# Kernel optimization log

Hardware: AMD Instinct MI355X
Metric: run time of the kernel (lower is better)

## Reference

```python
import jax, jax.numpy as jnp
import numpy as np

C_S = 256
C_Z = 128
C_HIDDEN = 32
NO_HEADS = 8
INF = 1000000000.0
EPS = 1e-5


def _layernorm(x, w, b):
    mu = jnp.mean(x, axis=-1, keepdims=True)
    var = jnp.var(x, axis=-1, keepdims=True)
    return (x - mu) * jax.lax.rsqrt(var + EPS) * w + b


def setup_inputs() -> dict:
    key = jax.random.key(0)
    ks = jax.random.split(key, 12)
    B, S, R = 1, 128, 256
    H, D = NO_HEADS, C_HIDDEN
    hd = H * D
    inp = {
        "s": jax.random.normal(ks[0], (B, S, R, C_S), dtype=jnp.float32),
        "z": jax.random.normal(ks[1], (B, R, R, C_Z), dtype=jnp.float32),
        "mask": jnp.ones((B, S, R), dtype=jnp.float32),
        "ln_s_w": jnp.ones((C_S,), dtype=jnp.float32),
        "ln_s_b": jnp.zeros((C_S,), dtype=jnp.float32),
        "ln_z_w": jnp.ones((C_Z,), dtype=jnp.float32),
        "ln_z_b": jnp.zeros((C_Z,), dtype=jnp.float32),
        "w_z": jax.random.normal(ks[2], (C_Z, H), dtype=jnp.float32) * 0.02,
        "w_q": jax.random.normal(ks[3], (C_S, hd), dtype=jnp.float32) * (1.0 / np.sqrt(C_S)),
        "w_k": jax.random.normal(ks[4], (C_S, hd), dtype=jnp.float32) * (1.0 / np.sqrt(C_S)),
        "w_v": jax.random.normal(ks[5], (C_S, hd), dtype=jnp.float32) * (1.0 / np.sqrt(C_S)),
        "w_g": jax.random.normal(ks[6], (C_S, hd), dtype=jnp.float32) * 0.02,
        "b_g": jnp.ones((hd,), dtype=jnp.float32),
        "w_o": jax.random.normal(ks[7], (hd, C_S), dtype=jnp.float32) * (1.0 / np.sqrt(hd)),
        "b_o": jnp.zeros((C_S,), dtype=jnp.float32),
    }
    return inp


def reference(s, z, mask, ln_s_w, ln_s_b, ln_z_w, ln_z_b, w_z, w_q, w_k, w_v, w_g, b_g, w_o, b_o):
    B, S, R, _ = s.shape
    H, D = NO_HEADS, C_HIDDEN

    s_n = _layernorm(s, ln_s_w, ln_s_b)                      # [B,S,R,C_s]
    # mask bias: [B, S, 1, 1, R]
    mask_bias = (INF * (mask - 1.0))[..., :, None, None, :]
    # pair bias: [B, 1, H, R, R]
    z_n = _layernorm(z, ln_z_w, ln_z_b)                      # [B,R,R,C_z]
    pair_bias = jnp.einsum("bqkc,ch->bhqk", z_n, w_z)[:, None]

    q = jnp.einsum("bsqc,cx->bsqx", s_n, w_q).reshape(B, S, R, H, D)
    k = jnp.einsum("bskc,cx->bskx", s_n, w_k).reshape(B, S, R, H, D)
    v = jnp.einsum("bskc,cx->bskx", s_n, w_v).reshape(B, S, R, H, D)
    q = q * (1.0 / np.sqrt(D))

    # attention logits: [B, S, H, R(q), R(k)]
    logits = jnp.einsum("bsqhd,bskhd->bshqk", q, k) + mask_bias + pair_bias
    attn = jax.nn.softmax(logits, axis=-1)
    o = jnp.einsum("bshqk,bskhd->bsqhd", attn, v).reshape(B, S, R, H * D)

    g = jax.nn.sigmoid(jnp.einsum("bsqc,cx->bsqx", s_n, w_g) + b_g)
    o = o * g
    out = jnp.einsum("bsqx,xc->bsqc", o, w_o) + b_o          # [B,S,R,C_s]
    return out
```

## Files before the change

kernel.cpp:

```cpp
#include <hip/hip_runtime.h>
#include <math.h>

#define CS 256
#define CZ 128
#define HEADS 8
#define DH 32
#define SDIM 128
#define RDIM 256
#define MROWS (SDIM*RDIM)
#define ZROWS (RDIM*RDIM)
#define EPSF 1e-5f
#define LOG2E 1.44269504088896340736f

typedef __attribute__((ext_vector_type(8))) short short8_t;
typedef __attribute__((ext_vector_type(4))) float f32x4;

__device__ __forceinline__ float waveReduceSum(float v) {
    #pragma unroll
    for (int off = 32; off > 0; off >>= 1) v += __shfl_xor(v, off, 64);
    return v;
}

__device__ __forceinline__ unsigned short f2bf(float f) {
    unsigned u = __float_as_uint(f);
    unsigned r = (u + 0x7fffu + ((u >> 16) & 1u)) >> 16;
    return (unsigned short)r;
}

__device__ __forceinline__ float bf2f(unsigned short u) {
    return __uint_as_float(((unsigned)u) << 16);
}

__device__ __forceinline__ float bflo(unsigned u) { return __uint_as_float(u << 16); }
__device__ __forceinline__ float bfhi(unsigned u) { return __uint_as_float(u & 0xffff0000u); }

__device__ __forceinline__ unsigned cvt_pk_bf16(float a, float b) {
    unsigned r;
    asm("v_cvt_pk_bf16_f32 %0, %1, %2" : "=v"(r) : "v"(a), "v"(b));
    return r;
}

__global__ __launch_bounds__(256) void ln_s_kernel(const float* __restrict__ s,
        const float* __restrict__ w, const float* __restrict__ b,
        unsigned short* __restrict__ snb) {
    int wid = threadIdx.x >> 6;
    int lane = threadIdx.x & 63;
    int row = blockIdx.x * 4 + wid;
    const float4 v = ((const float4*)(s + (size_t)row * CS))[lane];
    float sum = waveReduceSum(v.x + v.y + v.z + v.w);
    float sq  = waveReduceSum(v.x*v.x + v.y*v.y + v.z*v.z + v.w*v.w);
    float mean = sum * (1.f/CS);
    float var  = sq * (1.f/CS) - mean*mean;
    float rstd = rsqrtf(var + EPSF);
    const float4 wv = ((const float4*)w)[lane];
    const float4 bv = ((const float4*)b)[lane];
    ushort4 o;
    o.x = f2bf((v.x-mean)*rstd*wv.x + bv.x);
    o.y = f2bf((v.y-mean)*rstd*wv.y + bv.y);
    o.z = f2bf((v.z-mean)*rstd*wv.z + bv.z);
    o.w = f2bf((v.w-mean)*rstd*wv.w + bv.w);
    ((ushort4*)(snb + (size_t)row * CS))[lane] = o;
}

__global__ __launch_bounds__(256) void ln_z_pb_kernel(const float* __restrict__ z,
        const float* __restrict__ w, const float* __restrict__ b,
        const float* __restrict__ wz, unsigned short* __restrict__ pb) {
    int wid = threadIdx.x >> 6;
    int lane = threadIdx.x & 63;
    int row = blockIdx.x * 4 + wid;
    const float2 v = ((const float2*)(z + (size_t)row * CZ))[lane];
    float sum = waveReduceSum(v.x + v.y);
    float sq  = waveReduceSum(v.x*v.x + v.y*v.y);
    float mean = sum * (1.f/CZ);
    float var  = sq * (1.f/CZ) - mean*mean;
    float rstd = rsqrtf(var + EPSF);
    const float2 wv = ((const float2*)w)[lane];
    const float2 bv = ((const float2*)b)[lane];
    float n0 = (v.x-mean)*rstd*wv.x + bv.x;
    float n1 = (v.y-mean)*rstd*wv.y + bv.y;
    const float* wz0 = wz + (size_t)(lane*2) * HEADS;
    float ph[8];
    #pragma unroll
    for (int h = 0; h < 8; h++) ph[h] = n0*wz0[h] + n1*wz0[HEADS + h];
    #pragma unroll
    for (int h = 0; h < 8; h++) ph[h] = waveReduceSum(ph[h]);
    if (lane == 0) {
        #pragma unroll
        for (int h = 0; h < 8; h++)
            pb[(size_t)h*ZROWS + row] = f2bf(ph[h]);
    }
}

__global__ __launch_bounds__(256) void wconv_kernel(const float* __restrict__ wq,
        const float* __restrict__ wk, const float* __restrict__ wv,
        const float* __restrict__ wg, const float* __restrict__ wo,
        unsigned short* __restrict__ wtb, unsigned short* __restrict__ wot) {
    __shared__ float T[64][65];
    const int wi = blockIdx.z;
    const float* W = (wi==0)?wq:(wi==1)?wk:(wi==2)?wv:(wi==3)?wg:wo;
    unsigned short* O = (wi<4) ? (wtb + (size_t)wi*65536) : wot;
    const int bk = blockIdx.x * 64, bn = blockIdx.y * 64;
    const int tx = threadIdx.x & 63, tg = threadIdx.x >> 6;
    #pragma unroll
    for (int i = 0; i < 16; i++) {
        int r = tg*16 + i;
        T[r][tx] = W[(size_t)(bk+r)*256 + bn + tx];
    }
    __syncthreads();
    #pragma unroll
    for (int i = 0; i < 16; i++) {
        int r = tg*16 + i;
        O[(size_t)(bn+r)*256 + bk + tx] = f2bf(T[tx][r]);
    }
}

__global__ __launch_bounds__(256, 3) void qkvg_kernel(
        const unsigned short* __restrict__ snb,
        const unsigned short* __restrict__ wtb,
        const float* __restrict__ bg,
        unsigned short* __restrict__ qo, unsigned short* __restrict__ ko,
        unsigned short* __restrict__ vo, unsigned short* __restrict__ go) {
    __shared__ alignas(16) unsigned short As[128][64];
    __shared__ alignas(16) unsigned short Bs[128][64];
    const int bx = blockIdx.x;
    const int mblk = (bx & 7) * 32 + (bx >> 3);
    const int m0 = mblk * 128;
    const int n0 = blockIdx.y * 128;
    const int seg = n0 >> 8;
    const int nseg = n0 & 255;
    const unsigned short* wt = wtb + (size_t)seg * 65536;
    const int tid = threadIdx.x;
    const int lane = tid & 63, wid = tid >> 6;
    const int ln15 = lane & 15, g = lane >> 4;
    const int wr = wid >> 1, wc = wid & 1;
    f32x4 acc[4][4];
    #pragma unroll
    for (int i = 0; i < 4; i++)
        #pragma unroll
        for (int j = 0; j < 4; j++) acc[i][j] = (f32x4){0.f,0.f,0.f,0.f};

    for (int k0 = 0; k0 < 256; k0 += 64) {
        #pragma unroll
        for (int ci = 0; ci < 4; ci++) {
            int n = tid + ci*256;
            int r = n >> 3, sc = n & 7;
            int gc = (sc + r) & 7;
            const unsigned short* sA = &snb[(size_t)(m0+r)*256 + k0 + gc*8];
            const unsigned short* sB = &wt[(size_t)(nseg+r)*256 + k0 + gc*8];
            __builtin_amdgcn_global_load_lds(
                (const __attribute__((address_space(1))) unsigned int*)sA,
                (__attribute__((address_space(3))) unsigned int*)(&As[0][0] + (size_t)(wid*64 + ci*256)*8),
                16, 0, 0);
            __builtin_amdgcn_global_load_lds(
                (const __attribute__((address_space(1))) unsigned int*)sB,
                (__attribute__((address_space(3))) unsigned int*)(&Bs[0][0] + (size_t)(wid*64 + ci*256)*8),
                16, 0, 0);
        }
        __syncthreads();
        #pragma unroll
        for (int kk = 0; kk < 64; kk += 32) {
            short8_t a[4], b[4];
            #pragma unroll
            for (int i = 0; i < 4; i++) {
                int ga = (kk >> 3) + g;
                int ra = wr*64 + i*16 + ln15;
                int rb = wc*64 + i*16 + ln15;
                a[i] = *(const short8_t*)&As[ra][((ga - ra) & 7) * 8];
                b[i] = *(const short8_t*)&Bs[rb][((ga - rb) & 7) * 8];
            }
            #pragma unroll
            for (int i = 0; i < 4; i++)
                #pragma unroll
                for (int j = 0; j < 4; j++)
                    acc[i][j] = __builtin_amdgcn_mfma_f32_16x16x32_bf16(
                                    a[i], b[j], acc[i][j], 0, 0, 0);
        }
        __syncthreads();
    }
    #pragma unroll
    for (int i = 0; i < 4; i++) {
        #pragma unroll
        for (int r = 0; r < 4; r++) {
            int m = m0 + wr*64 + i*16 + g*4 + r;
            int ss = m >> 8, rr = m & 255;
            #pragma unroll
            for (int j = 0; j < 4; j++) {
                int col = n0 + wc*64 + j*16 + ln15;
                int lc = col & 255;
                int h = lc >> 5, d = lc & 31;
                float val = acc[i][j][r];
                size_t qidx = (((size_t)ss*HEADS + h)*RDIM + rr)*DH + d;
                if (seg == 0)      qo[qidx] = f2bf(val * 0.17677669529663687f);
                else if (seg == 1) ko[qidx] = f2bf(val);
                else if (seg == 2) vo[qidx] = f2bf(val);
                else {
                    float x = val + bg[lc];
                    go[(size_t)m*CS + lc] = f2bf(1.f / (1.f + expf(-x)));
                }
            }
        }
    }
}

__global__ __launch_bounds__(256, 2) void attn_kernel(
        const unsigned short* __restrict__ q, const unsigned short* __restrict__ k,
        const unsigned short* __restrict__ v, const unsigned short* __restrict__ pb,
        const float* __restrict__ mask, unsigned short* __restrict__ o) {
    __shared__ alignas(16) unsigned short Klds[256][40];
    __shared__ alignas(16) unsigned short Vtlds[32][264];
    __shared__ alignas(16) unsigned short PBpb[4][4096];
    __shared__ alignas(16) unsigned short Plds[4][16][72];
    __shared__ float masklds[256];

    const int sh = blockIdx.x;
    const int ss = sh >> 3, h = sh & 7;
    const int tid = threadIdx.x;
    const int lane = tid & 63, wid = tid >> 6;
    const int ln15 = lane & 15, g = lane >> 4;

    const unsigned short* kp = k + (size_t)sh * 8192;
    const unsigned short* vp = v + (size_t)sh * 8192;
    const unsigned short* pbh = pb + (size_t)h * ZROWS;
    unsigned short* pbw = &PBpb[wid][0];

    {
        const unsigned short* pbase = pbh + (size_t)(wid*64) * RDIM;
        #pragma unroll
        for (int j = 0; j < 8; j++) {
            int w = j*64 + lane;
            int n = w ^ ((w >> 5) & 7);
            const unsigned short* src = pbase + (n >> 5) * RDIM + (n & 31) * 8;
            __builtin_amdgcn_global_load_lds(
                (const __attribute__((address_space(1))) unsigned int*)src,
                (__attribute__((address_space(3))) unsigned int*)(pbw + j*512),
                16, 0, 0);
        }
    }

    #pragma unroll
    for (int i = 0; i < 4; i++) {
        int idx = tid + i*256;
        int row = idx >> 2, col = (idx & 3) * 8;
        short8_t kv8 = *(const short8_t*)&kp[(size_t)row*DH + col];
        short8_t vv8 = *(const short8_t*)&vp[(size_t)row*DH + col];
        *(short8_t*)&Klds[row][col] = kv8;
        #pragma unroll
        for (int e = 0; e < 8; e++)
            Vtlds[col+e][row] = (unsigned short)vv8[e];
    }
    masklds[tid] = 1e9f * (mask[(size_t)ss*RDIM + tid] - 1.f);

    short8_t qfr[4];
    {
        const unsigned short* qp = q + (size_t)sh * 8192;
        #pragma unroll
        for (int qt = 0; qt < 4; qt++)
            qfr[qt] = *(const short8_t*)&qp[(size_t)(wid*64 + qt*16 + ln15)*DH + g*8];
    }
    __syncthreads();

    #pragma unroll 1
    for (int qt = 0; qt < 4; qt++) {
        const int q0 = wid*64 + qt*16;
        f32x4 st[16];
        #pragma unroll
        for (int t = 0; t < 16; t++) {
            short8_t kf = *(const short8_t*)&Klds[t*16 + ln15][g*8];
            st[t] = __builtin_amdgcn_mfma_f32_16x16x32_bf16(
                        kf, qfr[qt], (f32x4){0.f,0.f,0.f,0.f}, 0, 0, 0);
        }
        asm volatile("s_waitcnt vmcnt(0)" ::: "memory");
        __builtin_amdgcn_sched_barrier(0);
        #pragma unroll
        for (int t = 0; t < 16; t++) {
            int n = ln15*32 + t*2 + (g >> 1);
            int m = n ^ (ln15 & 7);
            uint2 p2 = *(const uint2*)&pbw[m*8 + (g & 1)*4];
            float4 mk4 = *(const float4*)&masklds[t*16 + g*4];
            st[t][0] += bflo(p2.x) + mk4.x;
            st[t][1] += bfhi(p2.x) + mk4.y;
            st[t][2] += bflo(p2.y) + mk4.z;
            st[t][3] += bfhi(p2.y) + mk4.w;
        }
        float mx = -INFINITY;
        #pragma unroll
        for (int t = 0; t < 16; t++) {
            float a = fmaxf(fmaxf(st[t][0], st[t][1]), fmaxf(st[t][2], st[t][3]));
            mx = fmaxf(mx, a);
        }
        mx = fmaxf(mx, __shfl_xor(mx, 16, 64));
        mx = fmaxf(mx, __shfl_xor(mx, 32, 64));
        const float mxl = mx * LOG2E;
        float l = 0.f;
        #pragma unroll
        for (int t = 0; t < 16; t++) {
            #pragma unroll
            for (int r = 0; r < 4; r++) {
                float p = exp2f(fmaf(st[t][r], LOG2E, -mxl));
                st[t][r] = p;
                l += p;
            }
        }
        l += __shfl_xor(l, 16, 64);
        l += __shfl_xor(l, 32, 64);
        float inv = 1.f / l;
        if (qt < 3) {
            const unsigned short* pbase = pbh + (size_t)(q0 + 16) * RDIM;
            #pragma unroll
            for (int j = 0; j < 8; j++) {
                int w = j*64 + lane;
                int n = w ^ ((w >> 5) & 7);
                const unsigned short* src = pbase + (n >> 5) * RDIM + (n & 31) * 8;
                __builtin_amdgcn_global_load_lds(
                    (const __attribute__((address_space(1))) unsigned int*)src,
                    (__attribute__((address_space(3))) unsigned int*)(pbw + j*512),
                    16, 0, 0);
            }
        }
        f32x4 oacc[2];
        oacc[0] = (f32x4){0.f,0.f,0.f,0.f};
        oacc[1] = (f32x4){0.f,0.f,0.f,0.f};
        #pragma unroll
        for (int c = 0; c < 4; c++) {
            #pragma unroll
            for (int tc = 0; tc < 4; tc++) {
                int t = c*4 + tc;
                uint2 w;
                w.x = cvt_pk_bf16(st[t][0], st[t][1]);
                w.y = cvt_pk_bf16(st[t][2], st[t][3]);
                *(uint2*)&Plds[wid][ln15][tc*16 + g*4] = w;
            }
            #pragma unroll
            for (int ks = 0; ks < 2; ks++) {
                short8_t pfr = *(const short8_t*)&Plds[wid][ln15][ks*32 + g*8];
                #pragma unroll
                for (int dt = 0; dt < 2; dt++) {
                    short8_t vf = *(const short8_t*)&Vtlds[dt*16 + ln15][c*64 + ks*32 + g*8];
                    oacc[dt] = __builtin_amdgcn_mfma_f32_16x16x32_bf16(
                                   vf, pfr, oacc[dt], 0, 0, 0);
                }
            }
        }
        #pragma unroll
        for (int dt = 0; dt < 2; dt++) {
            uint2 w;
            w.x = cvt_pk_bf16(oacc[dt][0]*inv, oacc[dt][1]*inv);
            w.y = cvt_pk_bf16(oacc[dt][2]*inv, oacc[dt][3]*inv);
            *(uint2*)&Plds[wid][ln15][dt*16 + g*4] = w;
        }
        {
            int qr = lane >> 2, dc = (lane & 3) * 8;
            short8_t ov = *(const short8_t*)&Plds[wid][qr][dc];
            *(short8_t*)&o[((size_t)ss*RDIM + q0 + qr)*CS + h*DH + dc] = ov;
        }
    }
}

__global__ __launch_bounds__(256, 3) void outproj_kernel(
        const unsigned short* __restrict__ ob, const unsigned short* __restrict__ gb,
        const unsigned short* __restrict__ wot, const float* __restrict__ bo,
        float* __restrict__ out) {
    __shared__ alignas(16) unsigned short As[128][64];
    __shared__ alignas(16) unsigned short Bs[128][64];
    const int bx = blockIdx.x;
    const int mblk = (bx & 7) * 32 + (bx >> 3);
    const int m0 = mblk * 128;
    const int n0 = blockIdx.y * 128;
    const int tid = threadIdx.x;
    const int lane = tid & 63, wid = tid >> 6;
    const int ln15 = lane & 15, g = lane >> 4;
    const int wr = wid >> 1, wc = wid & 1;
    f32x4 acc[4][4];
    #pragma unroll
    for (int i = 0; i < 4; i++)
        #pragma unroll
        for (int j = 0; j < 4; j++) acc[i][j] = (f32x4){0.f,0.f,0.f,0.f};

    for (int k0 = 0; k0 < 256; k0 += 64) {
        #pragma unroll
        for (int ci = 0; ci < 4; ci++) {
            int n = tid + ci*256;
            int r = n >> 3, sc = n & 7;
            int gcb = (sc + r) & 7;
            const unsigned short* sB = &wot[(size_t)(n0+r)*256 + k0 + gcb*8];
            __builtin_amdgcn_global_load_lds(
                (const __attribute__((address_space(1))) unsigned int*)sB,
                (__attribute__((address_space(3))) unsigned int*)(&Bs[0][0] + (size_t)(wid*64 + ci*256)*8),
                16, 0, 0);
            int row = r, gc = sc;
            short8_t ov = *(const short8_t*)&ob[(size_t)(m0+row)*256 + k0 + gc*8];
            short8_t gv = *(const short8_t*)&gb[(size_t)(m0+row)*256 + k0 + gc*8];
            unsigned pr[4];
            #pragma unroll
            for (int e = 0; e < 4; e++) {
                float p0 = bf2f((unsigned short)ov[e*2+0]) * bf2f((unsigned short)gv[e*2+0]);
                float p1 = bf2f((unsigned short)ov[e*2+1]) * bf2f((unsigned short)gv[e*2+1]);
                pr[e] = cvt_pk_bf16(p0, p1);
            }
            *(uint4*)&As[row][((gc - row) & 7) * 8] = *(uint4*)pr;
        }
        __syncthreads();
        #pragma unroll
        for (int kk = 0; kk < 64; kk += 32) {
            short8_t a[4], b[4];
            #pragma unroll
            for (int i = 0; i < 4; i++) {
                int ga = (kk >> 3) + g;
                int ra = wr*64 + i*16 + ln15;
                int rb = wc*64 + i*16 + ln15;
                a[i] = *(const short8_t*)&As[ra][((ga - ra) & 7) * 8];
                b[i] = *(const short8_t*)&Bs[rb][((ga - rb) & 7) * 8];
            }
            #pragma unroll
            for (int i = 0; i < 4; i++)
                #pragma unroll
                for (int j = 0; j < 4; j++)
                    acc[i][j] = __builtin_amdgcn_mfma_f32_16x16x32_bf16(
                                    a[i], b[j], acc[i][j], 0, 0, 0);
        }
        __syncthreads();
    }
    #pragma unroll
    for (int i = 0; i < 4; i++) {
        #pragma unroll
        for (int r = 0; r < 4; r++) {
            int m = m0 + wr*64 + i*16 + g*4 + r;
            #pragma unroll
            for (int j = 0; j < 4; j++) {
                int col = n0 + wc*64 + j*16 + ln15;
                out[(size_t)m*CS + col] = acc[i][j][r] + bo[col];
            }
        }
    }
}

extern "C" void kernel_launch(void* const* d_in, const int* in_sizes, int n_in,
                              void* d_out, int out_size, void* d_ws, size_t ws_size,
                              hipStream_t stream) {
    const float* s      = (const float*)d_in[0];
    const float* z      = (const float*)d_in[1];
    const float* mask   = (const float*)d_in[2];
    const float* ln_s_w = (const float*)d_in[3];
    const float* ln_s_b = (const float*)d_in[4];
    const float* ln_z_w = (const float*)d_in[5];
    const float* ln_z_b = (const float*)d_in[6];
    const float* w_z    = (const float*)d_in[7];
    const float* w_q    = (const float*)d_in[8];
    const float* w_k    = (const float*)d_in[9];
    const float* w_v    = (const float*)d_in[10];
    const float* w_g    = (const float*)d_in[11];
    const float* b_g    = (const float*)d_in[12];
    const float* w_o    = (const float*)d_in[13];
    const float* b_o    = (const float*)d_in[14];
    float* out = (float*)d_out;
    float* ws  = (float*)d_ws;

    unsigned short* snb = (unsigned short*)ws;
    unsigned short* wtb = (unsigned short*)(ws + 4194304);
    unsigned short* wot = (unsigned short*)(ws + 4194304+131072);
    unsigned short* pbb = (unsigned short*)(ws + 4194304+131072+32768);
    float* after_pb = ws + 4194304 + 131072 + 32768 + 262144;
    unsigned short* qb  = (unsigned short*)after_pb;
    unsigned short* kb  = qb + 8388608;
    unsigned short* vb  = kb + 8388608;
    unsigned short* gbuf= vb + 8388608;
    unsigned short* obuf= gbuf + 8388608;

    ln_s_kernel<<<MROWS/4, 256, 0, stream>>>(s, ln_s_w, ln_s_b, snb);
    ln_z_pb_kernel<<<ZROWS/4, 256, 0, stream>>>(z, ln_z_w, ln_z_b, w_z, pbb);
    wconv_kernel<<<dim3(4,4,5), 256, 0, stream>>>(w_q, w_k, w_v, w_g, w_o, wtb, wot);
    qkvg_kernel<<<dim3(MROWS/128, 8), 256, 0, stream>>>(snb, wtb, b_g, qb, kb, vb, gbuf);
    attn_kernel<<<SDIM*HEADS, 256, 0, stream>>>(qb, kb, vb, pbb, mask, obuf);
    outproj_kernel<<<dim3(MROWS/128, 2), 256, 0, stream>>>(obuf, gbuf, wot, b_o, out);
}
```

Before: 174.3 us.

## Compute z pair-bias projection with MFMA and coalesced bf16 stores

Rewrites the z layernorm and pair-bias kernel so each block handles 64 rows. Each lane-group of 16 lanes owns one row, and the 128x8 projection runs as bf16 MFMA 16x16x32 instead of eight full-wave shuffle reductions per row. Results are staged in shared memory and written as 16-byte vector stores per head, replacing scattered 2-byte stores. This cuts shuffle traffic and store inefficiency, at the cost of rounding the normalized z and w_z to bf16 before the dot product.

```diff
diff --git a/kernel.cpp b/kernel.cpp
--- a/kernel.cpp
+++ b/kernel.cpp
@@ -65,29 +65,73 @@
 __global__ __launch_bounds__(256) void ln_z_pb_kernel(const float* __restrict__ z,
         const float* __restrict__ w, const float* __restrict__ b,
         const float* __restrict__ wz, unsigned short* __restrict__ pb) {
-    int wid = threadIdx.x >> 6;
-    int lane = threadIdx.x & 63;
-    int row = blockIdx.x * 4 + wid;
-    const float2 v = ((const float2*)(z + (size_t)row * CZ))[lane];
-    float sum = waveReduceSum(v.x + v.y);
-    float sq  = waveReduceSum(v.x*v.x + v.y*v.y);
+    __shared__ unsigned short Pol[8][64];
+    const int tid = threadIdx.x;
+    const int lane = tid & 63, wid = tid >> 6;
+    const int ln15 = lane & 15, g = lane >> 4;
+    const int base = blockIdx.x * 64;
+    const int row = base + wid*16 + ln15;
+    const float* zr = z + (size_t)row * CZ;
+
+    short8_t wzf[4];
+    #pragma unroll
+    for (int kk = 0; kk < 4; kk++) {
+        short8_t f;
+        #pragma unroll
+        for (int j = 0; j < 8; j++) {
+            float vv = (ln15 < 8) ? wz[(size_t)(kk*32 + g*8 + j)*HEADS + ln15] : 0.f;
+            f[j] = (short)f2bf(vv);
+        }
+        wzf[kk] = f;
+    }
+    float zv[4][8];
+    float sum = 0.f, sq = 0.f;
+    #pragma unroll
+    for (int kk = 0; kk < 4; kk++) {
+        float4 a0 = *(const float4*)&zr[kk*32 + g*8];
+        float4 a1 = *(const float4*)&zr[kk*32 + g*8 + 4];
+        zv[kk][0]=a0.x; zv[kk][1]=a0.y; zv[kk][2]=a0.z; zv[kk][3]=a0.w;
+        zv[kk][4]=a1.x; zv[kk][5]=a1.y; zv[kk][6]=a1.z; zv[kk][7]=a1.w;
+        #pragma unroll
+        for (int j = 0; j < 8; j++) { sum += zv[kk][j]; sq = fmaf(zv[kk][j], zv[kk][j], sq); }
+    }
+    sum += __shfl_xor(sum, 16, 64); sum += __shfl_xor(sum, 32, 64);
+    sq  += __shfl_xor(sq, 16, 64);  sq  += __shfl_xor(sq, 32, 64);
     float mean = sum * (1.f/CZ);
     float var  = sq * (1.f/CZ) - mean*mean;
     float rstd = rsqrtf(var + EPSF);
-    const float2 wv = ((const float2*)w)[lane];
-    const float2 bv = ((const float2*)b)[lane];
-    float n0 = (v.x-mean)*rstd*wv.x + bv.x;
-    float n1 = (v.y-mean)*rstd*wv.y + bv.y;
-    const float* wz0 = wz + (size_t)(lane*2) * HEADS;
-    float ph[8];
-    #pragma unroll
-    for (int h = 0; h < 8; h++) ph[h] = n0*wz0[h] + n1*wz0[HEADS + h];
-    #pragma unroll
-    for (int h = 0; h < 8; h++) ph[h] = waveReduceSum(ph[h]);
-    if (lane == 0) {
-        #pragma unroll
-        for (int h = 0; h < 8; h++)
-            pb[(size_t)h*ZROWS + row] = f2bf(ph[h]);
+    float mr = mean * rstd;
+    short8_t znf[4];
+    #pragma unroll
+    for (int kk = 0; kk < 4; kk++) {
+        float4 w0 = *(const float4*)&w[kk*32 + g*8];
+        float4 w1 = *(const float4*)&w[kk*32 + g*8 + 4];
+        float4 b0 = *(const float4*)&b[kk*32 + g*8];
+        float4 b1 = *(const float4*)&b[kk*32 + g*8 + 4];
+        float wl[8] = {w0.x,w0.y,w0.z,w0.w,w1.x,w1.y,w1.z,w1.w};
+        float bl[8] = {b0.x,b0.y,b0.z,b0.w,b1.x,b1.y,b1.z,b1.w};
+        unsigned pk[4];
+        #pragma unroll
+        for (int e = 0; e < 4; e++) {
+            float n0 = fmaf(fmaf(zv[kk][e*2+0], rstd, -mr), wl[e*2+0], bl[e*2+0]);
+            float n1 = fmaf(fmaf(zv[kk][e*2+1], rstd, -mr), wl[e*2+1], bl[e*2+1]);
+            pk[e] = cvt_pk_bf16(n0, n1);
+        }
+        znf[kk] = *(short8_t*)pk;
+    }
+    f32x4 acc = (f32x4){0.f,0.f,0.f,0.f};
+    #pragma unroll
+    for (int kk = 0; kk < 4; kk++)
+        acc = __builtin_amdgcn_mfma_f32_16x16x32_bf16(wzf[kk], znf[kk], acc, 0, 0, 0);
+    if (g < 2) {
+        #pragma unroll
+        for (int r = 0; r < 4; r++)
+            Pol[g*4 + r][wid*16 + ln15] = f2bf(acc[r]);
+    }
+    __syncthreads();
+    if (tid < 64) {
+        int h = tid >> 3, seg = tid & 7;
+        *(uint4*)&pb[(size_t)h*ZROWS + base + seg*8] = *(uint4*)&Pol[h][seg*8];
     }
 }
 
@@ -467,7 +511,7 @@
     unsigned short* obuf= gbuf + 8388608;
 
     ln_s_kernel<<<MROWS/4, 256, 0, stream>>>(s, ln_s_w, ln_s_b, snb);
-    ln_z_pb_kernel<<<ZROWS/4, 256, 0, stream>>>(z, ln_z_w, ln_z_b, w_z, pbb);
+    ln_z_pb_kernel<<<ZROWS/64, 256, 0, stream>>>(z, ln_z_w, ln_z_b, w_z, pbb);
     wconv_kernel<<<dim3(4,4,5), 256, 0, stream>>>(w_q, w_k, w_v, w_g, w_o, wtb, wot);
     qkvg_kernel<<<dim3(MROWS/128, 8), 256, 0, stream>>>(snb, wtb, b_g, qb, kb, vb, gbuf);
     attn_kernel<<<SDIM*HEADS, 256, 0, stream>>>(qb, kb, vb, pbb, mask, obuf);
```

New measurement: 143.4 us, median of 3. 1.22x faster.
